# Optimization experiments

Hardware: AMD Instinct MI355X
Metric: run time of the kernel (lower is better)

## Reference

```python
import jax, jax.numpy as jnp
from jax import lax
import numpy as np

# db4 filter bank (pywt convention): rec_lo is the canonical Daubechies-4 scaling filter
_REC_LO = np.array([0.23037781330885523, 0.7148465705525415, 0.6308807679295904,
                    -0.02798376941698385, -0.18703481171888114, 0.030841381835986965,
                    0.032883011666982945, -0.010597401784997278])
L = 8
_DEC_LO = _REC_LO[::-1].copy()
_DEC_HI = _REC_LO * ((-1.0) ** (np.arange(L) + 1))  # pywt dec_hi
_REC_HI = _DEC_HI[::-1].copy()
LEVEL = 2


def dwt_step(x):
    """Single-level DWT, pywt 'symmetric' mode. x: (N, S) -> a, d: (N, floor((S+L-1)/2))."""
    n, s = x.shape
    ext = jnp.pad(x, ((0, 0), (L - 1, L - 1)), mode='symmetric')[:, 1:]  # start at conv index 1
    # XLA conv is correlation; flip dec filters to get true convolution
    k = jnp.stack([_DEC_LO[::-1], _DEC_HI[::-1]]).astype(x.dtype)[:, None, :]  # (2,1,L)
    y = lax.conv_general_dilated(ext[:, None, :], k, window_strides=(2,), padding='VALID',
                                 dimension_numbers=('NCH', 'OIH', 'NCH'))  # (N,2,Lc)
    return y[:, 0], y[:, 1]


def idwt_step(a, d):
    """Single-level inverse DWT (pywt). Output length 2*la - L + 2."""
    la = a.shape[1]
    coef = jnp.stack([a, d], axis=1)  # (N,2,la)
    k = jnp.stack([_REC_LO[::-1], _REC_HI[::-1]]).astype(a.dtype)[None, :, :]  # (1,2,L) summed over a/d
    y = lax.conv_general_dilated(coef, k, window_strides=(1,), padding=[(L - 1, L - 1)],
                                 lhs_dilation=(2,),  # upsample-by-2 then full convolution
                                 dimension_numbers=('NCH', 'OIH', 'NCH'))  # (N,1,2la+L-2)
    return y[:, 0, L - 2: L - 2 + (2 * la - L + 2)]


def soft(c, t):
    return jnp.sign(c) * jnp.maximum(jnp.abs(c) - t, 0.0)


def denoise_2d(x2d):
    """x2d: (N, S) batch of signals; wavedec->soft-threshold->waverec, per-signal threshold."""
    s = x2d.shape[1]
    a = x2d
    details = []  # appended finest-first: [d1, d2]
    for _ in range(LEVEL):
        a, d = dwt_step(a)
        details.append(d)
    d1 = details[0]  # coeffs[-1] in pywt ordering = finest detail
    sigma = jnp.median(jnp.abs(d1), axis=1) / 0.6745
    thr = (sigma * jnp.sqrt(2.0 * jnp.log(jnp.asarray(s, x2d.dtype))))[:, None]
    rec = soft(a, thr)
    for d in details[::-1]:  # coarsest-first reconstruction
        d = soft(d, thr)
        rec = rec[:, : d.shape[1]]  # pywt waverec crops approx when one longer than detail
        rec = idwt_step(rec, d)
    return rec[:, :s]


def setup_inputs() -> dict:
    key = jax.random.key(0)
    x = jax.random.normal(key, (32, 8192, 64), dtype=jnp.float32)
    return {"x": x}


def reference(x):
    b, s, f = x.shape
    x2 = jnp.transpose(x, (0, 2, 1)).reshape(b * f, s)  # (B*F, S): every signal independent
    y = denoise_2d(x2)
    return y.reshape(b, f, s).transpose(0, 2, 1)
```

## Files before the change

kernel.cpp:

```cpp
#include <hip/hip_runtime.h>

#define S0LEN 8192
#define L1LEN 4099
#define L2LEN 2053
#define NROWS 2048
#define NTT   512
#define NT2   512

constexpr float DEC_LO[8] = {
  -0.010597401784997278f,  0.032883011666982945f,  0.030841381835986965f,
  -0.18703481171888114f,  -0.02798376941698385f,   0.6308807679295904f,
   0.7148465705525415f,    0.23037781330885523f };
constexpr float DEC_HI[8] = {
  -0.23037781330885523f,   0.7148465705525415f,   -0.6308807679295904f,
  -0.02798376941698385f,   0.18703481171888114f,   0.030841381835986965f,
  -0.032883011666982945f, -0.010597401784997278f };
constexpr float REC_LO[8] = {
   0.23037781330885523f,   0.7148465705525415f,    0.6308807679295904f,
  -0.02798376941698385f,  -0.18703481171888114f,   0.030841381835986965f,
   0.032883011666982945f, -0.010597401784997278f };
constexpr float REC_HI[8] = {
  -0.010597401784997278f, -0.032883011666982945f,  0.030841381835986965f,
   0.18703481171888114f,  -0.02798376941698385f,  -0.6308807679295904f,
   0.7148465705525415f,   -0.23037781330885523f };

__device__ __forceinline__ int refl(int m, int n) {
  m = (m < 0) ? (-1 - m) : m;
  m = (m >= n) ? (2 * n - 1 - m) : m;
  return m;
}

__device__ __forceinline__ float softf(float c, float t) {
  float m = fmaxf(fabsf(c) - t, 0.0f);
  return copysignf(m, c);
}

__device__ __forceinline__ void dwt_pair_vec(const float* __restrict__ buf,
                                             int e2, int e4a, int e4b,
                                             float& ae, float& de, float& ao, float& dd) {
  const float2 w01 = reinterpret_cast<const float2*>(buf)[e2];
  const float4 w25 = reinterpret_cast<const float4*>(buf)[e4a];
  const float4 w69 = reinterpret_cast<const float4*>(buf)[e4b];
  const float w[10] = {w01.x, w01.y, w25.x, w25.y, w25.z, w25.w,
                       w69.x, w69.y, w69.z, w69.w};
  ae = de = ao = dd = 0.f;
#pragma unroll
  for (int q = 0; q < 8; ++q) {
    ae = fmaf(DEC_LO[7 - q], w[q],     ae);
    de = fmaf(DEC_HI[7 - q], w[q],     de);
    ao = fmaf(DEC_LO[7 - q], w[q + 2], ao);
    dd = fmaf(DEC_HI[7 - q], w[q + 2], dd);
  }
}

__device__ __forceinline__ void dwt_scalar(const float* __restrict__ buf, int gbase,
                                           int i, int n, float& a, float& d) {
  a = d = 0.f;
#pragma unroll
  for (int q = 0; q < 8; ++q) {
    const float v = buf[refl(2 * i - 6 + q, n) - gbase];
    a = fmaf(DEC_LO[7 - q], v, a);
    d = fmaf(DEC_HI[7 - q], v, d);
  }
}

__device__ __forceinline__ float4 idwt_quad(const float* __restrict__ w,
                                            const float* __restrict__ v) {
  float4 o; float acc;
  acc = 0.f;
#pragma unroll
  for (int u = 0; u < 4; ++u) { acc = fmaf(w[3-u], REC_LO[2*u],   acc); acc = fmaf(v[3-u], REC_HI[2*u],   acc); }
  o.x = acc;
  acc = 0.f;
#pragma unroll
  for (int u = 0; u < 4; ++u) { acc = fmaf(w[3-u], REC_LO[2*u+1], acc); acc = fmaf(v[3-u], REC_HI[2*u+1], acc); }
  o.y = acc;
  acc = 0.f;
#pragma unroll
  for (int u = 0; u < 4; ++u) { acc = fmaf(w[4-u], REC_LO[2*u],   acc); acc = fmaf(v[4-u], REC_HI[2*u],   acc); }
  o.z = acc;
  acc = 0.f;
#pragma unroll
  for (int u = 0; u < 4; ++u) { acc = fmaf(w[4-u], REC_LO[2*u+1], acc); acc = fmaf(v[4-u], REC_HI[2*u+1], acc); }
  o.w = acc;
  return o;
}

__global__ void __launch_bounds__(NTT)
k_transpose_fwd(const float* __restrict__ x, float* __restrict__ xt) {
  const int b  = blockIdx.y;
  const int s0 = blockIdx.x * 256;
  __shared__ float tile[64][256];
  const int t = threadIdx.x;
  const int lane = t & 63;
  const int wv = t >> 6;

  const float* src = x + ((size_t)b * S0LEN + s0) * 64;
  float4 rg[8];
#pragma unroll
  for (int k = 0; k < 8; ++k)
    rg[k] = reinterpret_cast<const float4*>(src)[t + NTT * k];
#pragma unroll
  for (int k = 0; k < 8; ++k) {
    const int n  = t + NTT * k;
    const int s  = n >> 4;
    const int fg = n & 15;
    const int sc = s ^ (4 * (fg & 7));
    tile[4 * fg + 0][sc] = rg[k].x;
    tile[4 * fg + 1][sc] = rg[k].y;
    tile[4 * fg + 2][sc] = rg[k].z;
    tile[4 * fg + 3][sc] = rg[k].w;
  }
  __syncthreads();
#pragma unroll
  for (int j = 0; j < 8; ++j) {
    const int f = 8 * wv + j;
    const int swz = 4 * ((f >> 2) & 7);
    const float4 v = *reinterpret_cast<const float4*>(&tile[f][(4 * lane) ^ swz]);
    reinterpret_cast<float4*>(xt + (size_t)(b * 64 + f) * S0LEN + s0)[lane] = v;
  }
}

__global__ void __launch_bounds__(NT2, 6)
k_denoise(float* __restrict__ ws) {
  const int r = blockIdx.x;
  float* row = ws + (size_t)r * S0LEN;

  __shared__ alignas(16) float X[4112];
  __shared__ alignas(16) float A[4100];
  __shared__ alignas(16) float D[4100];
  __shared__ unsigned hist[1024];
  __shared__ unsigned wsum[4];
  __shared__ int sh_bin, sh_k;
  const int t = threadIdx.x;

  {
    const float4* s4 = reinterpret_cast<const float4*>(row);
    float4* d4 = reinterpret_cast<float4*>(X);
    for (int j = t; j < 1027; j += NT2) d4[j] = s4[j];
  }
  __syncthreads();

  for (int p = t; p < 1024; p += NT2) {
    float ae, de, ao, dd;
    if (p >= 2) dwt_pair_vec(X, 2 * p - 3, p - 1, p, ae, de, ao, dd);
    else { dwt_scalar(X, 0, 2 * p, S0LEN, ae, de); dwt_scalar(X, 0, 2 * p + 1, S0LEN, ao, dd); }
    reinterpret_cast<float2*>(A)[p] = make_float2(ae, ao);
    reinterpret_cast<float2*>(D)[p] = make_float2(de, dd);
  }
  __syncthreads();

  {
    const float4* s4 = reinterpret_cast<const float4*>(row) + 1022;
    float4* d4 = reinterpret_cast<float4*>(X);
    for (int j = t; j < 1026; j += NT2) d4[j] = s4[j];
  }
  __syncthreads();

  for (int p0 = t; p0 < 1025; p0 += NT2) {
    const int p = 1024 + p0;
    float ae, de, ao, dd;
    if (p < 2048) dwt_pair_vec(X, 2 * p - 2047, p - 1023, p - 1022, ae, de, ao, dd);
    else { dwt_scalar(X, 4088, 2 * p, S0LEN, ae, de); dwt_scalar(X, 4088, 2 * p + 1, S0LEN, ao, dd); }
    reinterpret_cast<float2*>(A)[p] = make_float2(ae, ao);
    reinterpret_cast<float2*>(D)[p] = make_float2(de, dd);
  }
  if (t == 0) {
    float a, d; dwt_scalar(X, 4088, 4098, S0LEN, a, d);
    A[4098] = a; D[4098] = d;
  }
  __syncthreads();

  for (int p = t; p < 1026; p += NT2) {
    float ae, de, ao, dd;
    if (p >= 2 && p <= 1023) dwt_pair_vec(A, 2 * p - 3, p - 1, p, ae, de, ao, dd);
    else { dwt_scalar(A, 0, 2 * p, L1LEN, ae, de); dwt_scalar(A, 0, 2 * p + 1, L1LEN, ao, dd); }
    reinterpret_cast<float2*>(X)[p] = make_float2(ae, ao);
    reinterpret_cast<float2*>(X)[1028 + p] = make_float2(de, dd);
  }
  if (t == 1) {
    float a, d; dwt_scalar(A, 0, 2052, L1LEN, a, d);
    X[2052] = a; X[2056 + 2052] = d;
  }
  __syncthreads();

  unsigned prefval = 0u, himask = 0u;
  int kk = 2049;
  for (int pass = 0; pass < 4; ++pass) {
    const int shift = 24 - 8 * pass;
    for (int i = t; i < 1024; i += NT2) hist[i] = 0u;
    __syncthreads();
    unsigned* myh = hist + ((t >> 7) << 8);
    for (int i = t; i < L1LEN; i += NT2) {
      const unsigned u = __float_as_uint(fabsf(D[i]));
      if ((u & himask) == prefval) atomicAdd(&myh[(u >> shift) & 255u], 1u);
    }
    __syncthreads();
    unsigned c = 0u, incl = 0u;
    if (t < 256) {
      c = hist[t] + hist[t + 256] + hist[t + 512] + hist[t + 768];
      incl = c;
#pragma unroll
      for (int dlt = 1; dlt < 64; dlt <<= 1) {
        const unsigned nn = __shfl_up(incl, dlt, 64);
        if ((t & 63) >= dlt) incl += nn;
      }
      if ((t & 63) == 63) wsum[t >> 6] = incl;
    }
    __syncthreads();
    if (t < 256) {
      unsigned base = 0u;
      for (int w = 0; w < (t >> 6); ++w) base += wsum[w];
      incl += base;
      if ((unsigned)kk < incl && (unsigned)kk >= incl - c) {
        sh_bin = t; sh_k = kk - (int)(incl - c);
      }
    }
    __syncthreads();
    prefval |= ((unsigned)sh_bin) << shift;
    himask  |= 255u << shift;
    kk = sh_k;
  }
  const float thr = (__uint_as_float(prefval) / 0.6745f) * sqrtf(2.0f * logf(8192.0f));

  {
    const float* a2 = X;
    const float* d2 = X + 2056;
    for (int q = t; q < 1024; q += NT2) {
      const float2 a0 = reinterpret_cast<const float2*>(a2)[q];
      const float2 a1 = reinterpret_cast<const float2*>(a2)[q + 1];
      const float  a4 = a2[2 * q + 4];
      const float2 b0 = reinterpret_cast<const float2*>(d2)[q];
      const float2 b1 = reinterpret_cast<const float2*>(d2)[q + 1];
      const float  b4 = d2[2 * q + 4];
      const float w[5] = {softf(a0.x, thr), softf(a0.y, thr), softf(a1.x, thr),
                          softf(a1.y, thr), softf(a4, thr)};
      const float v[5] = {softf(b0.x, thr), softf(b0.y, thr), softf(b1.x, thr),
                          softf(b1.y, thr), softf(b4, thr)};
      reinterpret_cast<float4*>(A)[q] = idwt_quad(w, v);
    }
    if (t < 3) {
      const int i = 4096 + t, p = i >> 1, oo = i & 1;
      float acc = 0.f;
#pragma unroll
      for (int u = 0; u < 4; ++u) {
        acc = fmaf(softf(a2[p + 3 - u], thr), REC_LO[2 * u + oo], acc);
        acc = fmaf(softf(d2[p + 3 - u], thr), REC_HI[2 * u + oo], acc);
      }
      A[i] = acc;
    }
  }
  __syncthreads();

  for (int q = t; q < 2048; q += NT2) {
    const float2 r0 = reinterpret_cast<const float2*>(A)[q];
    const float2 r1 = reinterpret_cast<const float2*>(A)[q + 1];
    const float  r4 = A[2 * q + 4];
    const float2 e0 = reinterpret_cast<const float2*>(D)[q];
    const float2 e1 = reinterpret_cast<const float2*>(D)[q + 1];
    const float  e4 = D[2 * q + 4];
    const float w[5] = {r0.x, r0.y, r1.x, r1.y, r4};
    const float v[5] = {softf(e0.x, thr), softf(e0.y, thr), softf(e1.x, thr),
                        softf(e1.y, thr), softf(e4, thr)};
    reinterpret_cast<float4*>(row)[q] = idwt_quad(w, v);
  }
}

__global__ void __launch_bounds__(NTT)
k_transpose_bwd(const float* __restrict__ xt, float* __restrict__ out) {
  const int b  = blockIdx.y;
  const int s0 = blockIdx.x * 256;
  __shared__ float tile[64][256];
  const int t = threadIdx.x;
  const int lane = t & 63;
  const int wv = t >> 6;

#pragma unroll
  for (int j = 0; j < 8; ++j) {
    const int f = 8 * wv + j;
    const int swz = 4 * ((f >> 2) & 7);
    const float4 v = reinterpret_cast<const float4*>(xt + (size_t)(b * 64 + f) * S0LEN + s0)[lane];
    *reinterpret_cast<float4*>(&tile[f][(4 * lane) ^ swz]) = v;
  }
  __syncthreads();

  float* dst = out + ((size_t)b * S0LEN + s0) * 64;
#pragma unroll
  for (int k = 0; k < 8; ++k) {
    const int n  = t + NTT * k;
    const int s  = n >> 4;
    const int fg = n & 15;
    const int sc = s ^ (4 * (fg & 7));
    float4 v;
    v.x = tile[4 * fg + 0][sc];
    v.y = tile[4 * fg + 1][sc];
    v.z = tile[4 * fg + 2][sc];
    v.w = tile[4 * fg + 3][sc];
    reinterpret_cast<float4*>(dst)[n] = v;
  }
}

extern "C" void kernel_launch(void* const* d_in, const int* in_sizes, int n_in,
                              void* d_out, int out_size, void* d_ws, size_t ws_size,
                              hipStream_t stream) {
  (void)in_sizes; (void)n_in; (void)out_size; (void)ws_size;
  const float* x = (const float*)d_in[0];
  float* out = (float*)d_out;
  float* ws  = (float*)d_ws;

  const dim3 gT(S0LEN / 256, 32);
  hipLaunchKernelGGL(k_transpose_fwd, gT, dim3(NTT), 0, stream, x, ws);
  hipLaunchKernelGGL(k_denoise, dim3(NROWS), dim3(NT2), 0, stream, ws);
  hipLaunchKernelGGL(k_transpose_bwd, gT, dim3(NTT), 0, stream, ws, out);
}
```

Before: 189.3 us.

## Fuse transposes into denoise kernel with strided global loads and stores

Removes the separate forward and backward transpose kernels and the workspace round trip. The denoise kernel now reads each signal directly from the (B,S,F) input with a stride of 64 floats and writes results back strided. Block indices are remapped so blocks sharing cache lines run near each other. This trades two full memory passes for uncoalesced per-element global accesses that rely on cache reuse across blocks.

New measurement: 293.2 us. +54.8%, slower.

```diff
diff --git a/kernel.cpp b/kernel.cpp
--- a/kernel.cpp
+++ b/kernel.cpp
@@ -4,7 +4,6 @@
 #define L1LEN 4099
 #define L2LEN 2053
 #define NROWS 2048
-#define NTT   512
 #define NT2   512
 
 constexpr float DEC_LO[8] = {
@@ -86,45 +85,13 @@
   return o;
 }
 
-__global__ void __launch_bounds__(NTT)
-k_transpose_fwd(const float* __restrict__ x, float* __restrict__ xt) {
-  const int b  = blockIdx.y;
-  const int s0 = blockIdx.x * 256;
-  __shared__ float tile[64][256];
-  const int t = threadIdx.x;
-  const int lane = t & 63;
-  const int wv = t >> 6;
-
-  const float* src = x + ((size_t)b * S0LEN + s0) * 64;
-  float4 rg[8];
-#pragma unroll
-  for (int k = 0; k < 8; ++k)
-    rg[k] = reinterpret_cast<const float4*>(src)[t + NTT * k];
-#pragma unroll
-  for (int k = 0; k < 8; ++k) {
-    const int n  = t + NTT * k;
-    const int s  = n >> 4;
-    const int fg = n & 15;
-    const int sc = s ^ (4 * (fg & 7));
-    tile[4 * fg + 0][sc] = rg[k].x;
-    tile[4 * fg + 1][sc] = rg[k].y;
-    tile[4 * fg + 2][sc] = rg[k].z;
-    tile[4 * fg + 3][sc] = rg[k].w;
-  }
-  __syncthreads();
-#pragma unroll
-  for (int j = 0; j < 8; ++j) {
-    const int f = 8 * wv + j;
-    const int swz = 4 * ((f >> 2) & 7);
-    const float4 v = *reinterpret_cast<const float4*>(&tile[f][(4 * lane) ^ swz]);
-    reinterpret_cast<float4*>(xt + (size_t)(b * 64 + f) * S0LEN + s0)[lane] = v;
-  }
-}
-
 __global__ void __launch_bounds__(NT2, 6)
-k_denoise(float* __restrict__ ws) {
-  const int r = blockIdx.x;
-  float* row = ws + (size_t)r * S0LEN;
+k_denoise_fused(const float* __restrict__ x, float* __restrict__ out) {
+  const int i   = blockIdx.x;
+  const int f   = (i >> 3) & 63;
+  const int b   = (i & 7) + 8 * (i >> 9);
+  const float* xg = x   + (size_t)b * S0LEN * 64 + f;
+  float*       og = out + (size_t)b * S0LEN * 64 + f;
 
   __shared__ alignas(16) float X[4112];
   __shared__ alignas(16) float A[4100];
@@ -134,11 +101,7 @@
   __shared__ int sh_bin, sh_k;
   const int t = threadIdx.x;
 
-  {
-    const float4* s4 = reinterpret_cast<const float4*>(row);
-    float4* d4 = reinterpret_cast<float4*>(X);
-    for (int j = t; j < 1027; j += NT2) d4[j] = s4[j];
-  }
+  for (int j = t; j < 4108; j += NT2) X[j] = xg[(size_t)j * 64];
   __syncthreads();
 
   for (int p = t; p < 1024; p += NT2) {
@@ -150,11 +113,7 @@
   }
   __syncthreads();
 
-  {
-    const float4* s4 = reinterpret_cast<const float4*>(row) + 1022;
-    float4* d4 = reinterpret_cast<float4*>(X);
-    for (int j = t; j < 1026; j += NT2) d4[j] = s4[j];
-  }
+  for (int j = t; j < 4104; j += NT2) X[j] = xg[(size_t)(4088 + j) * 64];
   __syncthreads();
 
   for (int p0 = t; p0 < 1025; p0 += NT2) {
@@ -188,11 +147,11 @@
   int kk = 2049;
   for (int pass = 0; pass < 4; ++pass) {
     const int shift = 24 - 8 * pass;
-    for (int i = t; i < 1024; i += NT2) hist[i] = 0u;
+    for (int j = t; j < 1024; j += NT2) hist[j] = 0u;
     __syncthreads();
     unsigned* myh = hist + ((t >> 7) << 8);
-    for (int i = t; i < L1LEN; i += NT2) {
-      const unsigned u = __float_as_uint(fabsf(D[i]));
+    for (int j = t; j < L1LEN; j += NT2) {
+      const unsigned u = __float_as_uint(fabsf(D[j]));
       if ((u & himask) == prefval) atomicAdd(&myh[(u >> shift) & 255u], 1u);
     }
     __syncthreads();
@@ -240,14 +199,14 @@
       reinterpret_cast<float4*>(A)[q] = idwt_quad(w, v);
     }
     if (t < 3) {
-      const int i = 4096 + t, p = i >> 1, oo = i & 1;
+      const int ii = 4096 + t, p = ii >> 1, oo = ii & 1;
       float acc = 0.f;
 #pragma unroll
       for (int u = 0; u < 4; ++u) {
         acc = fmaf(softf(a2[p + 3 - u], thr), REC_LO[2 * u + oo], acc);
         acc = fmaf(softf(d2[p + 3 - u], thr), REC_HI[2 * u + oo], acc);
       }
-      A[i] = acc;
+      A[ii] = acc;
     }
   }
   __syncthreads();
@@ -262,54 +221,18 @@
     const float w[5] = {r0.x, r0.y, r1.x, r1.y, r4};
     const float v[5] = {softf(e0.x, thr), softf(e0.y, thr), softf(e1.x, thr),
                         softf(e1.y, thr), softf(e4, thr)};
-    reinterpret_cast<float4*>(row)[q] = idwt_quad(w, v);
-  }
-}
-
-__global__ void __launch_bounds__(NTT)
-k_transpose_bwd(const float* __restrict__ xt, float* __restrict__ out) {
-  const int b  = blockIdx.y;
-  const int s0 = blockIdx.x * 256;
-  __shared__ float tile[64][256];
-  const int t = threadIdx.x;
-  const int lane = t & 63;
-  const int wv = t >> 6;
-
-#pragma unroll
-  for (int j = 0; j < 8; ++j) {
-    const int f = 8 * wv + j;
-    const int swz = 4 * ((f >> 2) & 7);
-    const float4 v = reinterpret_cast<const float4*>(xt + (size_t)(b * 64 + f) * S0LEN + s0)[lane];
-    *reinterpret_cast<float4*>(&tile[f][(4 * lane) ^ swz]) = v;
-  }
-  __syncthreads();
-
-  float* dst = out + ((size_t)b * S0LEN + s0) * 64;
-#pragma unroll
-  for (int k = 0; k < 8; ++k) {
-    const int n  = t + NTT * k;
-    const int s  = n >> 4;
-    const int fg = n & 15;
-    const int sc = s ^ (4 * (fg & 7));
-    float4 v;
-    v.x = tile[4 * fg + 0][sc];
-    v.y = tile[4 * fg + 1][sc];
-    v.z = tile[4 * fg + 2][sc];
-    v.w = tile[4 * fg + 3][sc];
-    reinterpret_cast<float4*>(dst)[n] = v;
+    const float4 o = idwt_quad(w, v);
+    float* p = og + (size_t)(4 * q) * 64;
+    p[0] = o.x; p[64] = o.y; p[128] = o.z; p[192] = o.w;
   }
 }
 
 extern "C" void kernel_launch(void* const* d_in, const int* in_sizes, int n_in,
                               void* d_out, int out_size, void* d_ws, size_t ws_size,
                               hipStream_t stream) {
-  (void)in_sizes; (void)n_in; (void)out_size; (void)ws_size;
+  (void)in_sizes; (void)n_in; (void)out_size; (void)d_ws; (void)ws_size;
   const float* x = (const float*)d_in[0];
   float* out = (float*)d_out;
-  float* ws  = (float*)d_ws;
-
-  const dim3 gT(S0LEN / 256, 32);
-  hipLaunchKernelGGL(k_transpose_fwd, gT, dim3(NTT), 0, stream, x, ws);
-  hipLaunchKernelGGL(k_denoise, dim3(NROWS), dim3(NT2), 0, stream, ws);
-  hipLaunchKernelGGL(k_transpose_bwd, gT, dim3(NTT), 0, stream, ws, out);
-}
+
+  hipLaunchKernelGGL(k_denoise_fused, dim3(NROWS), dim3(NT2), 0, stream, x, out);
+}
```

## Compute four DWT outputs per thread and histogram from registers

Applied to the files above, without the earlier changes.

Each thread now produces four approximation/detail outputs per DWT pass from wider float4 loads, and the inverse passes emit eight outputs per thread, which cuts shared-memory load instructions and loop overhead. The level-1 detail magnitudes are kept in registers for the radix-select median, so the histogram passes no longer reread D from LDS. The histogram, its scan scratch and the broadcast slots are moved into the A buffer, which frees static LDS and may improve occupancy. In exchange, register pressure rises, boundary handling is more intricate, and an extra barrier is needed before A is reused.

Measured after the change: 185.0 us. -2.3%, faster.

```diff
diff --git a/kernel.cpp b/kernel.cpp
--- a/kernel.cpp
+++ b/kernel.cpp
@@ -35,22 +35,28 @@
   return copysignf(m, c);
 }
 
-__device__ __forceinline__ void dwt_pair_vec(const float* __restrict__ buf,
-                                             int e2, int e4a, int e4b,
-                                             float& ae, float& de, float& ao, float& dd) {
-  const float2 w01 = reinterpret_cast<const float2*>(buf)[e2];
-  const float4 w25 = reinterpret_cast<const float4*>(buf)[e4a];
-  const float4 w69 = reinterpret_cast<const float4*>(buf)[e4b];
-  const float w[10] = {w01.x, w01.y, w25.x, w25.y, w25.z, w25.w,
-                       w69.x, w69.y, w69.z, w69.w};
-  ae = de = ao = dd = 0.f;
-#pragma unroll
-  for (int q = 0; q < 8; ++q) {
-    ae = fmaf(DEC_LO[7 - q], w[q],     ae);
-    de = fmaf(DEC_HI[7 - q], w[q],     de);
-    ao = fmaf(DEC_LO[7 - q], w[q + 2], ao);
-    dd = fmaf(DEC_HI[7 - q], w[q + 2], dd);
-  }
+__device__ __forceinline__ void dwt_quad_vec(const float* __restrict__ buf,
+                                             int e2, int e4,
+                                             float4& A4, float4& D4) {
+  const float2 v0 = reinterpret_cast<const float2*>(buf)[e2];
+  const float4 v1 = reinterpret_cast<const float4*>(buf)[e4];
+  const float4 v2 = reinterpret_cast<const float4*>(buf)[e4 + 1];
+  const float4 v3 = reinterpret_cast<const float4*>(buf)[e4 + 2];
+  const float w[14] = {v0.x, v0.y, v1.x, v1.y, v1.z, v1.w,
+                       v2.x, v2.y, v2.z, v2.w, v3.x, v3.y, v3.z, v3.w};
+  float a[4], d[4];
+#pragma unroll
+  for (int r = 0; r < 4; ++r) {
+    float aa = 0.f, dd = 0.f;
+#pragma unroll
+    for (int q = 0; q < 8; ++q) {
+      aa = fmaf(DEC_LO[7 - q], w[2 * r + q], aa);
+      dd = fmaf(DEC_HI[7 - q], w[2 * r + q], dd);
+    }
+    a[r] = aa; d[r] = dd;
+  }
+  A4 = make_float4(a[0], a[1], a[2], a[3]);
+  D4 = make_float4(d[0], d[1], d[2], d[3]);
 }
 
 __device__ __forceinline__ void dwt_scalar(const float* __restrict__ buf, int gbase,
@@ -129,10 +135,10 @@
   __shared__ alignas(16) float X[4112];
   __shared__ alignas(16) float A[4100];
   __shared__ alignas(16) float D[4100];
-  __shared__ unsigned hist[1024];
-  __shared__ unsigned wsum[4];
-  __shared__ int sh_bin, sh_k;
   const int t = threadIdx.x;
+
+  unsigned myu[8];
+  unsigned exU[3];
 
   {
     const float4* s4 = reinterpret_cast<const float4*>(row);
@@ -141,12 +147,21 @@
   }
   __syncthreads();
 
-  for (int p = t; p < 1024; p += NT2) {
-    float ae, de, ao, dd;
-    if (p >= 2) dwt_pair_vec(X, 2 * p - 3, p - 1, p, ae, de, ao, dd);
-    else { dwt_scalar(X, 0, 2 * p, S0LEN, ae, de); dwt_scalar(X, 0, 2 * p + 1, S0LEN, ao, dd); }
-    reinterpret_cast<float2*>(A)[p] = make_float2(ae, ao);
-    reinterpret_cast<float2*>(D)[p] = make_float2(de, dd);
+  {
+    float4 a4, d4;
+    if (t >= 1) {
+      dwt_quad_vec(X, 4 * t - 3, 2 * t - 1, a4, d4);
+    } else {
+      float av[4], dv[4];
+#pragma unroll
+      for (int i = 0; i < 4; ++i) dwt_scalar(X, 0, i, S0LEN, av[i], dv[i]);
+      a4 = make_float4(av[0], av[1], av[2], av[3]);
+      d4 = make_float4(dv[0], dv[1], dv[2], dv[3]);
+    }
+    reinterpret_cast<float4*>(A)[t] = a4;
+    reinterpret_cast<float4*>(D)[t] = d4;
+    myu[0] = __float_as_uint(fabsf(d4.x)); myu[1] = __float_as_uint(fabsf(d4.y));
+    myu[2] = __float_as_uint(fabsf(d4.z)); myu[3] = __float_as_uint(fabsf(d4.w));
   }
   __syncthreads();
 
@@ -157,88 +172,115 @@
   }
   __syncthreads();
 
-  for (int p0 = t; p0 < 1025; p0 += NT2) {
-    const int p = 1024 + p0;
-    float ae, de, ao, dd;
-    if (p < 2048) dwt_pair_vec(X, 2 * p - 2047, p - 1023, p - 1022, ae, de, ao, dd);
-    else { dwt_scalar(X, 4088, 2 * p, S0LEN, ae, de); dwt_scalar(X, 4088, 2 * p + 1, S0LEN, ao, dd); }
-    reinterpret_cast<float2*>(A)[p] = make_float2(ae, ao);
-    reinterpret_cast<float2*>(D)[p] = make_float2(de, dd);
-  }
-  if (t == 0) {
-    float a, d; dwt_scalar(X, 4088, 4098, S0LEN, a, d);
-    A[4098] = a; D[4098] = d;
-  }
-  __syncthreads();
-
-  for (int p = t; p < 1026; p += NT2) {
-    float ae, de, ao, dd;
-    if (p >= 2 && p <= 1023) dwt_pair_vec(A, 2 * p - 3, p - 1, p, ae, de, ao, dd);
-    else { dwt_scalar(A, 0, 2 * p, L1LEN, ae, de); dwt_scalar(A, 0, 2 * p + 1, L1LEN, ao, dd); }
-    reinterpret_cast<float2*>(X)[p] = make_float2(ae, ao);
-    reinterpret_cast<float2*>(X)[1028 + p] = make_float2(de, dd);
-  }
-  if (t == 1) {
-    float a, d; dwt_scalar(A, 0, 2052, L1LEN, a, d);
-    X[2052] = a; X[2056 + 2052] = d;
-  }
-  __syncthreads();
-
+  {
+    float4 a4, d4;
+    dwt_quad_vec(X, 4 * t + 1, 2 * t + 1, a4, d4);
+    reinterpret_cast<float4*>(A)[512 + t] = a4;
+    reinterpret_cast<float4*>(D)[512 + t] = d4;
+    myu[4] = __float_as_uint(fabsf(d4.x)); myu[5] = __float_as_uint(fabsf(d4.y));
+    myu[6] = __float_as_uint(fabsf(d4.z)); myu[7] = __float_as_uint(fabsf(d4.w));
+    if (t == 0) {
+#pragma unroll
+      for (int i = 0; i < 3; ++i) {
+        float av, dv;
+        dwt_scalar(X, 4088, 4096 + i, S0LEN, av, dv);
+        A[4096 + i] = av; D[4096 + i] = dv;
+        exU[i] = __float_as_uint(fabsf(dv));
+      }
+    }
+  }
+  __syncthreads();
+
+  {
+    float4 a4, d4;
+    if (t >= 1) {
+      dwt_quad_vec(A, 4 * t - 3, 2 * t - 1, a4, d4);
+    } else {
+      float av[4], dv[4];
+#pragma unroll
+      for (int i = 0; i < 4; ++i) dwt_scalar(A, 0, i, L1LEN, av[i], dv[i]);
+      a4 = make_float4(av[0], av[1], av[2], av[3]);
+      d4 = make_float4(dv[0], dv[1], dv[2], dv[3]);
+    }
+    reinterpret_cast<float4*>(X)[t] = a4;
+    reinterpret_cast<float4*>(X)[514 + t] = d4;
+    if (t == 1) {
+      for (int i = 2048; i <= 2052; ++i) {
+        float av, dv;
+        dwt_scalar(A, 0, i, L1LEN, av, dv);
+        X[i] = av; X[2056 + i] = dv;
+      }
+    }
+  }
+  __syncthreads();
+
+  unsigned* H = reinterpret_cast<unsigned*>(A);
   unsigned prefval = 0u, himask = 0u;
   int kk = 2049;
   for (int pass = 0; pass < 4; ++pass) {
     const int shift = 24 - 8 * pass;
-    for (int i = t; i < 1024; i += NT2) hist[i] = 0u;
+    reinterpret_cast<uint4*>(H)[t] = make_uint4(0u, 0u, 0u, 0u);
     __syncthreads();
-    unsigned* myh = hist + ((t >> 7) << 8);
-    for (int i = t; i < L1LEN; i += NT2) {
-      const unsigned u = __float_as_uint(fabsf(D[i]));
+    unsigned* myh = H + ((t >> 6) << 8);
+#pragma unroll
+    for (int s = 0; s < 8; ++s) {
+      const unsigned u = myu[s];
       if ((u & himask) == prefval) atomicAdd(&myh[(u >> shift) & 255u], 1u);
+    }
+    if (t == 0) {
+#pragma unroll
+      for (int s = 0; s < 3; ++s) {
+        const unsigned u = exU[s];
+        if ((u & himask) == prefval) atomicAdd(&myh[(u >> shift) & 255u], 1u);
+      }
     }
     __syncthreads();
     unsigned c = 0u, incl = 0u;
     if (t < 256) {
-      c = hist[t] + hist[t + 256] + hist[t + 512] + hist[t + 768];
+#pragma unroll
+      for (int w = 0; w < 8; ++w) c += H[(w << 8) + t];
       incl = c;
 #pragma unroll
       for (int dlt = 1; dlt < 64; dlt <<= 1) {
         const unsigned nn = __shfl_up(incl, dlt, 64);
         if ((t & 63) >= dlt) incl += nn;
       }
-      if ((t & 63) == 63) wsum[t >> 6] = incl;
+      if ((t & 63) == 63) H[2048 + (t >> 6)] = incl;
     }
     __syncthreads();
     if (t < 256) {
       unsigned base = 0u;
-      for (int w = 0; w < (t >> 6); ++w) base += wsum[w];
+      for (int w = 0; w < (t >> 6); ++w) base += H[2048 + w];
       incl += base;
       if ((unsigned)kk < incl && (unsigned)kk >= incl - c) {
-        sh_bin = t; sh_k = kk - (int)(incl - c);
+        H[2052] = (unsigned)t;
+        H[2053] = (unsigned)(kk - (int)(incl - c));
       }
     }
     __syncthreads();
-    prefval |= ((unsigned)sh_bin) << shift;
+    prefval |= H[2052] << shift;
     himask  |= 255u << shift;
-    kk = sh_k;
+    kk = (int)H[2053];
   }
   const float thr = (__uint_as_float(prefval) / 0.6745f) * sqrtf(2.0f * logf(8192.0f));
+  __syncthreads();
 
   {
     const float* a2 = X;
     const float* d2 = X + 2056;
-    for (int q = t; q < 1024; q += NT2) {
-      const float2 a0 = reinterpret_cast<const float2*>(a2)[q];
-      const float2 a1 = reinterpret_cast<const float2*>(a2)[q + 1];
-      const float  a4 = a2[2 * q + 4];
-      const float2 b0 = reinterpret_cast<const float2*>(d2)[q];
-      const float2 b1 = reinterpret_cast<const float2*>(d2)[q + 1];
-      const float  b4 = d2[2 * q + 4];
-      const float w[5] = {softf(a0.x, thr), softf(a0.y, thr), softf(a1.x, thr),
-                          softf(a1.y, thr), softf(a4, thr)};
-      const float v[5] = {softf(b0.x, thr), softf(b0.y, thr), softf(b1.x, thr),
-                          softf(b1.y, thr), softf(b4, thr)};
-      reinterpret_cast<float4*>(A)[q] = idwt_quad(w, v);
-    }
+    const float4 wa0 = reinterpret_cast<const float4*>(a2)[t];
+    const float4 wa1 = reinterpret_cast<const float4*>(a2)[t + 1];
+    const float4 wd0 = reinterpret_cast<const float4*>(d2)[t];
+    const float4 wd1 = reinterpret_cast<const float4*>(d2)[t + 1];
+    const float w[7] = {softf(wa0.x, thr), softf(wa0.y, thr), softf(wa0.z, thr),
+                        softf(wa0.w, thr), softf(wa1.x, thr), softf(wa1.y, thr),
+                        softf(wa1.z, thr)};
+    const float v[7] = {softf(wd0.x, thr), softf(wd0.y, thr), softf(wd0.z, thr),
+                        softf(wd0.w, thr), softf(wd1.x, thr), softf(wd1.y, thr),
+                        softf(wd1.z, thr)};
+    const float4 o0 = idwt_quad(w, v);
+    const float4 o1 = idwt_quad(w + 2, v + 2);
+    float tv = 0.f;
     if (t < 3) {
       const int i = 4096 + t, p = i >> 1, oo = i & 1;
       float acc = 0.f;
@@ -247,22 +289,27 @@
         acc = fmaf(softf(a2[p + 3 - u], thr), REC_LO[2 * u + oo], acc);
         acc = fmaf(softf(d2[p + 3 - u], thr), REC_HI[2 * u + oo], acc);
       }
-      A[i] = acc;
-    }
-  }
-  __syncthreads();
-
-  for (int q = t; q < 2048; q += NT2) {
-    const float2 r0 = reinterpret_cast<const float2*>(A)[q];
-    const float2 r1 = reinterpret_cast<const float2*>(A)[q + 1];
-    const float  r4 = A[2 * q + 4];
-    const float2 e0 = reinterpret_cast<const float2*>(D)[q];
-    const float2 e1 = reinterpret_cast<const float2*>(D)[q + 1];
-    const float  e4 = D[2 * q + 4];
-    const float w[5] = {r0.x, r0.y, r1.x, r1.y, r4};
-    const float v[5] = {softf(e0.x, thr), softf(e0.y, thr), softf(e1.x, thr),
-                        softf(e1.y, thr), softf(e4, thr)};
-    reinterpret_cast<float4*>(row)[q] = idwt_quad(w, v);
+      tv = acc;
+    }
+    reinterpret_cast<float4*>(A)[2 * t]     = o0;
+    reinterpret_cast<float4*>(A)[2 * t + 1] = o1;
+    if (t < 3) A[4096 + t] = tv;
+  }
+  __syncthreads();
+
+#pragma unroll
+  for (int mm = 0; mm < 2; ++mm) {
+    const int m = t + mm * 512;
+    const float4 wa0 = reinterpret_cast<const float4*>(A)[m];
+    const float4 wa1 = reinterpret_cast<const float4*>(A)[m + 1];
+    const float4 wd0 = reinterpret_cast<const float4*>(D)[m];
+    const float4 wd1 = reinterpret_cast<const float4*>(D)[m + 1];
+    const float w[7] = {wa0.x, wa0.y, wa0.z, wa0.w, wa1.x, wa1.y, wa1.z};
+    const float v[7] = {softf(wd0.x, thr), softf(wd0.y, thr), softf(wd0.z, thr),
+                        softf(wd0.w, thr), softf(wd1.x, thr), softf(wd1.y, thr),
+                        softf(wd1.z, thr)};
+    reinterpret_cast<float4*>(row)[2 * m]     = idwt_quad(w, v);
+    reinterpret_cast<float4*>(row)[2 * m + 1] = idwt_quad(w + 2, v + 2);
   }
 }
 
```
